# Kernel optimization log

Hardware: AMD Instinct MI355X
Metric: run time of the kernel (lower is better)

## Reference

```python
import jax, jax.numpy as jnp
import numpy as np
import math
from jax.scipy.special import gammaln

B, H, W = 32, 960, 960
BLOCK = 96  # official NIQE/NRQM block size

# AGGD shape-parameter lookup table (same grid as torch impl: 0.2..10 step 0.001)
_GAM_NP = np.arange(0.2, 10.0 + 1e-6, 0.001, dtype=np.float64)
_RG_NP = np.array([math.exp(2.0 * math.lgamma(2.0 / g) - math.lgamma(1.0 / g) - math.lgamma(3.0 / g)) for g in _GAM_NP], dtype=np.float32)
GAM = jnp.asarray(_GAM_NP.astype(np.float32))
RGAM = jnp.asarray(_RG_NP)

def _gauss_kernel(size, sigma):
    ax = np.arange(size, dtype=np.float64) - (size - 1) / 2.0
    xx, yy = np.meshgrid(ax, ax)
    k = np.exp(-(xx ** 2 + yy ** 2) / (2.0 * sigma ** 2))
    return (k / k.sum()).astype(np.float32)

K7 = jnp.asarray(_gauss_kernel(7, 7.0 / 6.0))[None, None]  # MSCN window
K3 = jnp.asarray(_gauss_kernel(3, 0.5))[None, None]        # pyramid / downsample kernel

def _conv_same(x, k, edge_pad):
    ph = k.shape[-1] // 2
    mode = 'edge' if edge_pad else 'constant'
    x = jnp.pad(x, ((0, 0), (0, 0), (ph, ph), (ph, ph)), mode=mode)
    return jax.lax.conv_general_dilated(x, k, (1, 1), 'VALID', dimension_numbers=('NCHW', 'OIHW', 'NCHW'))

def _normalize(img):
    # MSCN: (img - mu) / (sigma + 1), replicate padding
    mu = _conv_same(img, K7, True)
    sigma = jnp.sqrt(jnp.abs(_conv_same(img * img, K7, True) - mu * mu))
    return (img - mu) / (sigma + 1.0)

def _downsample(img):
    # gaussian blur (3x3, sigma 0.5, zero same-pad) + stride-2 decimation
    return _conv_same(img, K3, False)[:, :, ::2, ::2]

def _aggd(x):
    # x: [b, nb, h, w]; vectorized AGGD parameter estimation over all blocks
    hw = (-2, -1)
    x2 = x * x
    ml = (x < 0).astype(x.dtype)
    mr = (x > 0).astype(x.dtype)
    cl = jnp.maximum(ml.sum(hw), 1.0)
    cr = jnp.maximum(mr.sum(hw), 1.0)
    lstd = jnp.sqrt((x2 * ml).sum(hw) / cl)
    rstd = jnp.sqrt((x2 * mr).sum(hw) / cr)
    gh = lstd / jnp.maximum(rstd, 1e-12)
    rhat = jnp.mean(jnp.abs(x), hw) ** 2 / jnp.maximum(jnp.mean(x2, hw), 1e-12)
    rhn = rhat * (gh ** 3 + 1.0) * (gh + 1.0) / ((gh * gh + 1.0) ** 2)
    idx = jnp.argmin(jnp.abs(RGAM - rhn[..., None]), axis=-1)  # table lookup
    alpha = GAM[idx]
    conv = jnp.exp(0.5 * (gammaln(1.0 / alpha) - gammaln(3.0 / alpha)))
    return alpha, lstd * conv, rstd * conv

def _features(blocks):
    # 18 features per block: AGGD of block + AGGD of 4 shifted products
    alpha, bl, br = _aggd(blocks)
    feats = [alpha, (bl + br) / 2.0]
    for shift in ((0, 1), (1, 0), (1, 1), (1, -1)):
        sb = jnp.roll(blocks, shift, axis=(2, 3))
        a, l, r = _aggd(blocks * sb)
        mean = (r - l) * jnp.exp(gammaln(2.0 / a) - gammaln(1.0 / a))
        feats += [a, mean, l, r]
    return jnp.stack(feats, axis=-1)  # [b, nb, 18]

def _blocks(x, bs):
    b, _, h, w = x.shape
    nh, nw = h // bs, w // bs
    x = x[:, 0].reshape(b, nh, bs, nw, bs).transpose(0, 1, 3, 2, 4)
    return x.reshape(b, nh * nw, bs, bs)

def setup_inputs() -> dict:
    key = jax.random.key(0)
    k1, k2, k3 = jax.random.split(key, 3)
    X = jax.random.uniform(k1, (B, 1, H, W), jnp.float32) * 255.0
    mu_pris = jax.random.normal(k2, (36,), jnp.float32)
    A = jax.random.normal(k3, (36, 36), jnp.float32)
    cov_pris = A @ A.T / 36.0 + jnp.eye(36, dtype=jnp.float32)  # SPD pristine covariance
    return {"X": X, "mu_pris": mu_pris, "cov_pris": cov_pris}

def reference(X, mu_pris, cov_pris):
    feats = []
    img = X
    for scale in (1, 2):
        xn = _normalize(img)
        feats.append(_features(_blocks(xn, BLOCK // scale)))  # [b, 100, 18]
        if scale == 1:
            img = _downsample(img)
    d = jnp.concatenate(feats, axis=-1)  # [b, nb, 36]
    mu_dist = d.mean(axis=1)  # [b, 36]
    c = d - mu_dist[:, None, :]
    cov_dist = jnp.einsum('bnf,bng->bfg', c, c) / (d.shape[1] - 1)
    invcov = jnp.linalg.pinv((cov_pris[None] + cov_dist) / 2.0)
    diff = mu_pris[None] - mu_dist
    q = jnp.einsum('bf,bfg,bg->b', diff, invcov, diff)
    return jnp.sqrt(jnp.maximum(q, 0.0))
```

## Files before the change

kernel.cpp:

```cpp
#include <hip/hip_runtime.h>
#include <hip/hip_fp16.h>
#include <math.h>

#define NTAB 9801
typedef unsigned int uint;
typedef float f2v __attribute__((ext_vector_type(2)));
typedef _Float16 h2v __attribute__((ext_vector_type(2)));

struct WParams { float w1[7]; float wd[3]; };

__device__ inline __half2 u2h2(uint u) { return __builtin_bit_cast(__half2, u); }
__device__ inline float flo(uint u) { return __low2float(u2h2(u)); }
__device__ inline float fhi(uint u) { return __high2float(u2h2(u)); }
__device__ inline uint pkmul(uint a, uint b) { return __builtin_bit_cast(uint, __hmul2(u2h2(a), u2h2(b))); }
__device__ inline uint pack2(float a, float b) {
    return __builtin_bit_cast(uint, __builtin_amdgcn_cvt_pkrtz(a, b));
}
__device__ inline uint algn16(uint hi, uint lo) {
    return (uint)((((unsigned long long)hi << 32) | lo) >> 16);
}
__device__ inline float fdot2f(uint a, uint b, float c) {
    return __builtin_amdgcn_fdot2(__builtin_bit_cast(h2v, a), __builtin_bit_cast(h2v, b), c, false);
}
__device__ inline float rcpf(float x) { return __builtin_amdgcn_rcpf(x); }

template <int S, bool FUSE_DOWN, bool TABLES, typename TIN>
__global__ __launch_bounds__(256, 6) void mscn_col_k(const TIN* __restrict__ src,
                                                     uint* __restrict__ xn_out,
                                                     __half* __restrict__ down_out,
                                                     WParams wp,
                                                     float* __restrict__ rgam,
                                                     float* __restrict__ gam) {
    constexpr int ROW_W = 132, H_OUT = 42, H_IN = H_OUT + 6, RPT = H_OUT / 2;
    constexpr int NTX = (S + 255) / 256, NTY = (S + H_OUT - 1) / H_OUT;
    constexpr int NBLK = 32 * NTX * NTY;

    if constexpr (TABLES) {
        if (blockIdx.x >= (unsigned)NBLK) {
            int i = (blockIdx.x - NBLK) * 256 + threadIdx.x;
            if (i < NTAB) {
                double g = 0.2 + (double)i * 0.001;
                double v = exp(2.0 * lgamma(2.0 / g) - lgamma(1.0 / g) - lgamma(3.0 / g));
                rgam[i] = (float)v;
                gam[i]  = (float)g;
            }
            return;
        }
    }

    __shared__ uint tin[ROW_W * H_IN];

    const int tid = threadIdx.x;
    const int bid = blockIdx.x;
    const int b  = bid / (NTX * NTY);
    const int t2 = bid % (NTX * NTY);
    const int x0 = min((t2 / NTY) * 256, S - 256);
    const int y0 = min((t2 % NTY) * H_OUT, S - H_OUT);

    const float* w1 = wp.w1;
    uint wA[4], wB[4];
    wA[0] = pack2(0.f, w1[0]);   wA[1] = pack2(w1[1], w1[2]);
    wA[2] = pack2(w1[3], w1[4]); wA[3] = pack2(w1[5], w1[6]);
    wB[0] = pack2(w1[0], w1[1]); wB[1] = pack2(w1[2], w1[3]);
    wB[2] = pack2(w1[4], w1[5]); wB[3] = pack2(w1[6], 0.f);

    const TIN* img = src + (size_t)b * S * S;
    const bool interior = (x0 >= 4) && (x0 <= S - 260) && (y0 >= 3) && (y0 <= S - H_IN + 3);

    if (interior && sizeof(TIN) == 4) {
        const float4* base = reinterpret_cast<const float4*>((const float*)img + (size_t)(y0 - 3) * S + (x0 - 4));
        const int f4row = S / 4;
        for (int i = tid; i < 66 * H_IN; i += 256) {
            int r = i / 66, k = i - r * 66;
            float4 v = base[(size_t)r * f4row + k];
            tin[r * ROW_W + 2 * k]     = pack2(v.x, v.y);
            tin[r * ROW_W + 2 * k + 1] = pack2(v.z, v.w);
        }
    } else {
        for (int i = tid; i < ROW_W * H_IN; i += 256) {
            int r = i / ROW_W, w = i - r * ROW_W;
            int gy = y0 + r - 3; gy = gy < 0 ? 0 : (gy >= S ? S - 1 : gy);
            int c0 = x0 - 4 + 2 * w; c0 = c0 < 0 ? 0 : (c0 >= S ? S - 1 : c0);
            int c1 = x0 - 3 + 2 * w; c1 = c1 < 0 ? 0 : (c1 >= S ? S - 1 : c1);
            const TIN* rp = img + (size_t)gy * S;
            tin[i] = pack2((float)rp[c0], (float)rp[c1]);
        }
    }
    __syncthreads();

    const int g = tid >> 7, c = tid & 127;
    const int R0 = g * RPT;

    auto horiz = [&](int row, f2v& o1, f2v& o2) {
        const uint* pw = &tin[row * ROW_W + c];
        uint q0 = pw[0], q1 = pw[1], q2 = pw[2], q3 = pw[3], q4 = pw[4];
        uint p0 = pkmul(q0, q0), p1 = pkmul(q1, q1), p2 = pkmul(q2, q2),
             p3 = pkmul(q3, q3), p4 = pkmul(q4, q4);
        float s1A = fdot2f(q3, wA[3], fdot2f(q2, wA[2], fdot2f(q1, wA[1], fdot2f(q0, wA[0], 0.f))));
        float s2A = fdot2f(p3, wA[3], fdot2f(p2, wA[2], fdot2f(p1, wA[1], fdot2f(p0, wA[0], 0.f))));
        float s1B = fdot2f(q4, wB[3], fdot2f(q3, wB[2], fdot2f(q2, wB[1], fdot2f(q1, wB[0], 0.f))));
        float s2B = fdot2f(p4, wB[3], fdot2f(p3, wB[2], fdot2f(p2, wB[1], fdot2f(p1, wB[0], 0.f))));
        o1 = (f2v){s1A, s1B};
        o2 = (f2v){s2A, s2B};
    };

    f2v r1[7], r2[7];
#pragma unroll
    for (int ir = 0; ir < 6; ir++) horiz(R0 + ir, r1[ir], r2[ir]);

    uint* xnp = xn_out + ((((size_t)b * S + y0 + R0) * S + x0) >> 1) + c;
#pragma unroll
    for (int u = 0; u < RPT; u++) {
        horiz(R0 + u + 6, r1[(u + 6) % 7], r2[(u + 6) % 7]);
        f2v a1 = (f2v)(0.f), a2 = (f2v)(0.f);
#pragma unroll
        for (int dy = 0; dy < 7; dy++) {
            a1 += r1[(u + dy) % 7] * w1[dy];
            a2 += r2[(u + dy) % 7] * w1[dy];
        }
        uint qc = tin[(R0 + u + 3) * ROW_W + c + 2];
        float v0a = flo(qc), v0b = fhi(qc);
        float xa = (v0a - a1.x) * rcpf(sqrtf(fabsf(a2.x - a1.x * a1.x)) + 1.f);
        float xb = (v0b - a1.y) * rcpf(sqrtf(fabsf(a2.y - a1.y * a1.y)) + 1.f);
        xnp[(size_t)u * (S / 2)] = pack2(xa, xb);
    }

    if constexpr (FUSE_DOWN) {
        const float* wd = wp.wd;
        const int d = tid & 127, hf = tid >> 7;
        const int Xd = x0 / 2 + d;
        const float mL = (x0 + 2 * d - 1 >= 0) ? 1.f : 0.f;
#pragma unroll
        for (int jj = 0; jj <= RPT / 2; jj++) {
            int j = 2 * jj + hf;
            if (j >= RPT) continue;
            int Yd = y0 / 2 + j;
            float acc = 0.f;
#pragma unroll
            for (int a = 0; a < 3; a++) {
                int gy = 2 * Yd - 1 + a;
                if (gy < 0) continue;
                int tr = gy - y0 + 3;
                uint u1 = tin[tr * ROW_W + d + 1];
                uint u2 = tin[tr * ROW_W + d + 2];
                float rs = wd[0] * fhi(u1) * mL + wd[1] * flo(u2) + wd[2] * fhi(u2);
                acc += wd[a] * rs;
            }
            down_out[((size_t)b * (S / 2) + Yd) * (S / 2) + Xd] = __float2half(acc);
        }
    }
}

template <int BS>
__global__ __launch_bounds__(256) void feat2_k(const __half* __restrict__ xnimg, int S,
                                               const float* __restrict__ rgam,
                                               const float* __restrict__ gam,
                                               float* __restrict__ dfeat, int foff) {
    constexpr int WROW = BS / 2;
    constexpr int NWORD = BS * BS / 2;
    constexpr int NITER = (NWORD + 255) / 256;
    __shared__ uint xs[NWORD];
    __shared__ float red[4 * 20];
    __shared__ float tot[20];

    const int tid = threadIdx.x;
    const int b   = blockIdx.x / 100;
    const int blk = blockIdx.x % 100;
    const int by  = (blk / 10) * BS;
    const int bx  = (blk % 10) * BS;

    const uint* gw = (const uint*)xnimg;
    for (int i = tid; i < NWORD; i += 256) {
        int y = i / WROW, w = i - y * WROW;
        xs[i] = gw[((((size_t)b * S + by + y) * S + bx) >> 1) + w];
    }
    __syncthreads();

    float ssq[5], sab[5], ssg[5];
    uint  cnt[5];
#pragma unroll
    for (int v = 0; v < 5; v++) { ssq[v] = sab[v] = ssg[v] = 0.f; cnt[v] = 0u; }

    const uint ONE2 = 0x3C003C00u;

    for (int k = 0; k < NITER; k++) {
        int idx = tid + k * 256;
        if (idx * 2 < BS * BS) {
            int p0 = idx * 2;
            int y = p0 / BS;
            int x = p0 - y * BS;
            int w0i = x >> 1;
            int wm = w0i ? w0i - 1 : WROW - 1;
            int wp = (w0i + 1 == WROW) ? 0 : w0i + 1;
            int ym1 = y ? y - 1 : BS - 1;
            int rb = y * WROW, rbm = ym1 * WROW;
            uint V0 = xs[rb + w0i];
            uint WL = xs[rb + wm];
            uint AL = xs[rbm + wm];
            uint AC = xs[rbm + w0i];
            uint AR = xs[rbm + wp];
            uint vv[5];
            vv[0] = V0;
            vv[1] = pkmul(V0, algn16(V0, WL));
            vv[2] = pkmul(V0, AC);
            vv[3] = pkmul(V0, algn16(AC, AL));
            vv[4] = pkmul(V0, algn16(AR, AC));
#pragma unroll
            for (int v = 0; v < 5; v++) {
                uint av = vv[v] & 0x7FFF7FFFu;
                ssq[v] = fdot2f(vv[v], vv[v], ssq[v]);
                sab[v] = fdot2f(av, ONE2, sab[v]);
                ssg[v] = fdot2f(vv[v], av, ssg[v]);
                cnt[v] += (vv[v] >> 15) & 0x00010001u;
            }
        }
    }

    const int wid = tid >> 6, lane = tid & 63;
#pragma unroll
    for (int v = 0; v < 5; v++) {
        float a = ssq[v], bb = sab[v], cc = ssg[v];
        float dd = (float)((cnt[v] & 0xFFFFu) + (cnt[v] >> 16));
        for (int off = 32; off >= 1; off >>= 1) {
            a += __shfl_down(a, off); bb += __shfl_down(bb, off);
            cc += __shfl_down(cc, off); dd += __shfl_down(dd, off);
        }
        if (lane == 0) {
            red[wid * 20 + v]      = a;
            red[wid * 20 + 5 + v]  = bb;
            red[wid * 20 + 10 + v] = cc;
            red[wid * 20 + 15 + v] = dd;
        }
    }
    __syncthreads();
    if (tid < 20) tot[tid] = red[tid] + red[20 + tid] + red[40 + tid] + red[60 + tid];
    __syncthreads();

    if (tid < 5) {
        const int v = tid;
        const float N = (float)(BS * BS);
        float ssqv = tot[v], sabv = tot[5 + v], ssgv = tot[10 + v], clv = tot[15 + v];
        float sql = fmaxf(0.5f * (ssqv - ssgv), 0.f);
        float sqr = fmaxf(0.5f * (ssqv + ssgv), 0.f);
        float cl = fmaxf(clv, 1.f), cr = fmaxf(N - clv, 1.f);
        float lstd = sqrtf(sql / cl), rstd = sqrtf(sqr / cr);
        float gh = lstd / fmaxf(rstd, 1e-12f);
        float mabs = sabv / N, msq = ssqv / N;
        float rhat = (mabs * mabs) / fmaxf(msq, 1e-12f);
        float gh2 = gh * gh;
        float target = rhat * (gh * gh2 + 1.f) * (gh + 1.f) / ((gh2 + 1.f) * (gh2 + 1.f));

        int lo = 0, hi = NTAB - 1, j = NTAB;
        while (lo <= hi) {
            int mid = (lo + hi) >> 1;
            if (rgam[mid] >= target) { j = mid; hi = mid - 1; } else lo = mid + 1;
        }
        int i0 = j > 0 ? j - 1 : 0;
        int i1 = j < NTAB ? j : NTAB - 1;
        float d0 = fabsf(rgam[i0] - target);
        float d1 = fabsf(rgam[i1] - target);
        int bi = (d1 < d0) ? i1 : i0;

        float alpha = gam[bi];
        float conv  = expf(0.5f * (lgammaf(1.f / alpha) - lgammaf(3.f / alpha)));
        float bl = lstd * conv, br = rstd * conv;
        float* outp = dfeat + ((size_t)b * 100 + blk) * 36 + foff;
        if (v == 0) {
            outp[0] = alpha;
            outp[1] = 0.5f * (bl + br);
        } else {
            float mean = (br - bl) * expf(lgammaf(2.f / alpha) - lgammaf(1.f / alpha));
            int base = 2 + (v - 1) * 4;
            outp[base + 0] = alpha; outp[base + 1] = mean;
            outp[base + 2] = bl;    outp[base + 3] = br;
        }
    }
}

__global__ __launch_bounds__(256) void final_k(const float* __restrict__ dfeat,
                                               const float* __restrict__ mu_pris,
                                               const float* __restrict__ cov_pris,
                                               float* __restrict__ out) {
    __shared__ float  ds[3600];
    __shared__ float  mu[36];
    __shared__ double M[36][37];
    __shared__ double rhs[36];
    __shared__ double qacc;
    const int b = blockIdx.x, tid = threadIdx.x;
    const float* src = dfeat + (size_t)b * 3600;
    for (int i = tid; i < 3600; i += 256) ds[i] = src[i];
    __syncthreads();
    if (tid < 36) {
        float s = 0.f;
        for (int n = 0; n < 100; n++) s += ds[n * 36 + tid];
        mu[tid] = s / 100.f;
    }
    __syncthreads();
    for (int i = tid; i < 3600; i += 256) ds[i] -= mu[i % 36];
    if (tid < 36) rhs[tid] = (double)mu_pris[tid] - (double)mu[tid];
    if (tid == 0) qacc = 0.0;
    __syncthreads();
    for (int e = tid; e < 1296; e += 256) {
        int f = e / 36, g = e % 36;
        float s = 0.f;
        for (int n = 0; n < 100; n++) s += ds[n * 36 + f] * ds[n * 36 + g];
        M[f][g] = 0.5 * ((double)cov_pris[e] + (double)(s / 99.f));
    }
    __syncthreads();
    for (int j = 0; j < 36; j++) {
        if (tid == 0) qacc += rhs[j] * rhs[j] / M[j][j];
        int i = j + 1 + tid;
        if (i < 36) {
            double L = M[i][j] / M[j][j];
            for (int k = j; k < 36; k++) M[i][k] -= L * M[j][k];
            rhs[i] -= L * rhs[j];
        }
        __syncthreads();
    }
    if (tid == 0) out[b] = sqrtf((float)(qacc > 0.0 ? qacc : 0.0));
}

static WParams make_weights() {
    WParams p;
    double wt[7], s = 0.0; const double sg = 7.0 / 6.0;
    for (int i = 0; i < 7; i++) { double d = i - 3; wt[i] = exp(-d * d / (2.0 * sg * sg)); s += wt[i]; }
    for (int i = 0; i < 7; i++) p.w1[i] = (float)(wt[i] / s);
    double e1 = exp(-2.0), sd = 1.0 + 2.0 * e1;
    p.wd[0] = p.wd[2] = (float)(e1 / sd);
    p.wd[1] = (float)(1.0 / sd);
    return p;
}

extern "C" void kernel_launch(void* const* d_in, const int* in_sizes, int n_in,
                              void* d_out, int out_size, void* d_ws, size_t ws_size,
                              hipStream_t stream) {
    const float* X        = (const float*)d_in[0];
    const float* mu_pris  = (const float*)d_in[1];
    const float* cov_pris = (const float*)d_in[2];
    float* out = (float*)d_out;

    char* ws = (char*)d_ws;
    float*  rgam   = (float*)(ws);
    float*  gam    = (float*)(ws + 39424);
    float*  dfeat  = (float*)(ws + 78848);
    __half* xn960  = (__half*)(ws + 539648);
    __half* img480 = (__half*)(ws + 59522048);
    __half* xn480  = (__half*)(ws + 74267648);

    WParams wp = make_weights();

    constexpr int NB960 = 32 * 4 * 23;
    constexpr int TBLB  = (NTAB + 255) / 256;
    mscn_col_k<960, true,  true,  float ><<<NB960 + TBLB, 256, 0, stream>>>(
        X, (uint*)xn960, img480, wp, rgam, gam);
    mscn_col_k<480, false, false, __half><<<32 * 2 * 12, 256, 0, stream>>>(
        img480, (uint*)xn480, nullptr, wp, rgam, gam);
    feat2_k<96><<<3200, 256, 0, stream>>>(xn960, 960, rgam, gam, dfeat, 0);
    feat2_k<48><<<3200, 256, 0, stream>>>(xn480, 480, rgam, gam, dfeat, 18);
    final_k<<<32, 256, 0, stream>>>(dfeat, mu_pris, cov_pris, out);
}
```

Before: 223.2 us.

## Merge scale-2 MSCN with scale-1 features into one launch and vectorize loads

Refactors the MSCN and feature kernels into device bodies. The 480-scale MSCN and the 96-block feature extraction now share one launch, so independent work overlaps and one kernel boundary disappears. The MSCN tile height drops from 42 to 28 rows, raising block count and occupancy at the cost of more halo rows. Shared-memory stores and global loads are widened to uint2/uint4, the half-precision input path copies packed words directly, and the feature loop handles two words per thread. Heterogeneous blocks in the merged launch may balance unevenly.

```diff
diff --git a/kernel.cpp b/kernel.cpp
--- a/kernel.cpp
+++ b/kernel.cpp
@@ -24,34 +24,16 @@
 }
 __device__ inline float rcpf(float x) { return __builtin_amdgcn_rcpf(x); }
 
-template <int S, bool FUSE_DOWN, bool TABLES, typename TIN>
-__global__ __launch_bounds__(256, 6) void mscn_col_k(const TIN* __restrict__ src,
-                                                     uint* __restrict__ xn_out,
-                                                     __half* __restrict__ down_out,
-                                                     WParams wp,
-                                                     float* __restrict__ rgam,
-                                                     float* __restrict__ gam) {
-    constexpr int ROW_W = 132, H_OUT = 42, H_IN = H_OUT + 6, RPT = H_OUT / 2;
+template <int S, bool FUSE_DOWN, typename TIN>
+__device__ __forceinline__ void mscn_body(int bid, uint* tin,
+                                          const TIN* __restrict__ src,
+                                          uint* __restrict__ xn_out,
+                                          __half* __restrict__ down_out,
+                                          const WParams& wp) {
+    constexpr int ROW_W = 132, H_OUT = 28, H_IN = H_OUT + 6, RPT = H_OUT / 2;
     constexpr int NTX = (S + 255) / 256, NTY = (S + H_OUT - 1) / H_OUT;
-    constexpr int NBLK = 32 * NTX * NTY;
-
-    if constexpr (TABLES) {
-        if (blockIdx.x >= (unsigned)NBLK) {
-            int i = (blockIdx.x - NBLK) * 256 + threadIdx.x;
-            if (i < NTAB) {
-                double g = 0.2 + (double)i * 0.001;
-                double v = exp(2.0 * lgamma(2.0 / g) - lgamma(1.0 / g) - lgamma(3.0 / g));
-                rgam[i] = (float)v;
-                gam[i]  = (float)g;
-            }
-            return;
-        }
-    }
-
-    __shared__ uint tin[ROW_W * H_IN];
 
     const int tid = threadIdx.x;
-    const int bid = blockIdx.x;
     const int b  = bid / (NTX * NTY);
     const int t2 = bid % (NTX * NTY);
     const int x0 = min((t2 / NTY) * 256, S - 256);
@@ -67,23 +49,41 @@
     const TIN* img = src + (size_t)b * S * S;
     const bool interior = (x0 >= 4) && (x0 <= S - 260) && (y0 >= 3) && (y0 <= S - H_IN + 3);
 
-    if (interior && sizeof(TIN) == 4) {
-        const float4* base = reinterpret_cast<const float4*>((const float*)img + (size_t)(y0 - 3) * S + (x0 - 4));
-        const int f4row = S / 4;
-        for (int i = tid; i < 66 * H_IN; i += 256) {
-            int r = i / 66, k = i - r * 66;
-            float4 v = base[(size_t)r * f4row + k];
-            tin[r * ROW_W + 2 * k]     = pack2(v.x, v.y);
-            tin[r * ROW_W + 2 * k + 1] = pack2(v.z, v.w);
+    if constexpr (sizeof(TIN) == 4) {
+        if (interior) {
+            const float4* base = reinterpret_cast<const float4*>(
+                (const float*)img + (size_t)(y0 - 3) * S + (x0 - 4));
+            const int f4row = S / 4;
+            for (int i = tid; i < 66 * H_IN; i += 256) {
+                int r = i / 66, k = i - r * 66;
+                float4 v = base[(size_t)r * f4row + k];
+                uint2 pr; pr.x = pack2(v.x, v.y); pr.y = pack2(v.z, v.w);
+                *(uint2*)&tin[r * ROW_W + 2 * k] = pr;
+            }
+        } else {
+            for (int i = tid; i < ROW_W * H_IN; i += 256) {
+                int r = i / ROW_W, w = i - r * ROW_W;
+                int gy = y0 + r - 3; gy = gy < 0 ? 0 : (gy >= S ? S - 1 : gy);
+                int c0 = x0 - 4 + 2 * w; int c0c = c0 < 0 ? 0 : (c0 >= S ? S - 1 : c0);
+                int c1 = c0 + 1;         int c1c = c1 < 0 ? 0 : (c1 >= S ? S - 1 : c1);
+                const TIN* rp = img + (size_t)gy * S;
+                tin[i] = pack2((float)rp[c0c], (float)rp[c1c]);
+            }
         }
     } else {
+        const uint* gw = (const uint*)img;
         for (int i = tid; i < ROW_W * H_IN; i += 256) {
             int r = i / ROW_W, w = i - r * ROW_W;
             int gy = y0 + r - 3; gy = gy < 0 ? 0 : (gy >= S ? S - 1 : gy);
-            int c0 = x0 - 4 + 2 * w; c0 = c0 < 0 ? 0 : (c0 >= S ? S - 1 : c0);
-            int c1 = x0 - 3 + 2 * w; c1 = c1 < 0 ? 0 : (c1 >= S ? S - 1 : c1);
-            const TIN* rp = img + (size_t)gy * S;
-            tin[i] = pack2((float)rp[c0], (float)rp[c1]);
+            int c0 = x0 - 4 + 2 * w;
+            if (c0 >= 0 && c0 + 1 < S) {
+                tin[i] = gw[((size_t)gy * S + c0) >> 1];
+            } else {
+                int c0c = c0 < 0 ? 0 : (c0 >= S ? S - 1 : c0);
+                int c1c = (c0 + 1) < 0 ? 0 : ((c0 + 1) >= S ? S - 1 : c0 + 1);
+                const TIN* rp = img + (size_t)gy * S;
+                tin[i] = pack2((float)rp[c0c], (float)rp[c1c]);
+            }
         }
     }
     __syncthreads();
@@ -131,9 +131,8 @@
         const int Xd = x0 / 2 + d;
         const float mL = (x0 + 2 * d - 1 >= 0) ? 1.f : 0.f;
 #pragma unroll
-        for (int jj = 0; jj <= RPT / 2; jj++) {
+        for (int jj = 0; jj < RPT / 2; jj++) {
             int j = 2 * jj + hf;
-            if (j >= RPT) continue;
             int Yd = y0 / 2 + j;
             float acc = 0.f;
 #pragma unroll
@@ -152,27 +151,29 @@
 }
 
 template <int BS>
-__global__ __launch_bounds__(256) void feat2_k(const __half* __restrict__ xnimg, int S,
-                                               const float* __restrict__ rgam,
-                                               const float* __restrict__ gam,
-                                               float* __restrict__ dfeat, int foff) {
+__device__ __forceinline__ void feat2_body(int bid, uint* xs, float* red, float* tot,
+                                           const __half* __restrict__ xnimg, int S,
+                                           const float* __restrict__ rgam,
+                                           const float* __restrict__ gam,
+                                           float* __restrict__ dfeat, int foff) {
     constexpr int WROW = BS / 2;
     constexpr int NWORD = BS * BS / 2;
-    constexpr int NITER = (NWORD + 255) / 256;
-    __shared__ uint xs[NWORD];
-    __shared__ float red[4 * 20];
-    __shared__ float tot[20];
+    constexpr int PAIRS = NWORD / 2;
+    constexpr int PPR = WROW / 2;
 
     const int tid = threadIdx.x;
-    const int b   = blockIdx.x / 100;
-    const int blk = blockIdx.x % 100;
+    const int b   = bid / 100;
+    const int blk = bid % 100;
     const int by  = (blk / 10) * BS;
     const int bx  = (blk % 10) * BS;
 
     const uint* gw = (const uint*)xnimg;
-    for (int i = tid; i < NWORD; i += 256) {
-        int y = i / WROW, w = i - y * WROW;
-        xs[i] = gw[((((size_t)b * S + by + y) * S + bx) >> 1) + w];
+    uint4* xs4 = (uint4*)xs;
+    constexpr int NW4 = NWORD / 4;
+    constexpr int W4R = WROW / 4;
+    for (int i = tid; i < NW4; i += 256) {
+        int y = i / W4R, k = i - y * W4R;
+        xs4[i] = *(const uint4*)&gw[((((size_t)b * S + by + y) * S + bx) >> 1) + 4 * k];
     }
     __syncthreads();
 
@@ -183,35 +184,36 @@
 
     const uint ONE2 = 0x3C003C00u;
 
-    for (int k = 0; k < NITER; k++) {
+    for (int k = 0; k < (PAIRS + 255) / 256; k++) {
         int idx = tid + k * 256;
-        if (idx * 2 < BS * BS) {
-            int p0 = idx * 2;
-            int y = p0 / BS;
-            int x = p0 - y * BS;
-            int w0i = x >> 1;
-            int wm = w0i ? w0i - 1 : WROW - 1;
-            int wp = (w0i + 1 == WROW) ? 0 : w0i + 1;
-            int ym1 = y ? y - 1 : BS - 1;
-            int rb = y * WROW, rbm = ym1 * WROW;
-            uint V0 = xs[rb + w0i];
-            uint WL = xs[rb + wm];
-            uint AL = xs[rbm + wm];
-            uint AC = xs[rbm + w0i];
-            uint AR = xs[rbm + wp];
-            uint vv[5];
-            vv[0] = V0;
-            vv[1] = pkmul(V0, algn16(V0, WL));
-            vv[2] = pkmul(V0, AC);
-            vv[3] = pkmul(V0, algn16(AC, AL));
-            vv[4] = pkmul(V0, algn16(AR, AC));
+        if (idx < PAIRS) {
+            int y  = idx / PPR;
+            int pr = idx - y * PPR;
+            int w0 = pr * 2;
+            int rb = y * WROW, rbm = (y ? y - 1 : BS - 1) * WROW;
+            uint2 V = *(const uint2*)&xs[rb + w0];
+            uint WL  = xs[rb  + (w0 ? w0 - 1 : WROW - 1)];
+            uint2 A = *(const uint2*)&xs[rbm + w0];
+            uint AL  = xs[rbm + (w0 ? w0 - 1 : WROW - 1)];
+            uint AR  = xs[rbm + ((w0 + 2 == WROW) ? 0 : w0 + 2)];
+            uint vA[5], vB[5];
+            vA[0] = V.x;
+            vA[1] = pkmul(V.x, algn16(V.x, WL));
+            vA[2] = pkmul(V.x, A.x);
+            vA[3] = pkmul(V.x, algn16(A.x, AL));
+            vA[4] = pkmul(V.x, algn16(A.y, A.x));
+            vB[0] = V.y;
+            vB[1] = pkmul(V.y, algn16(V.y, V.x));
+            vB[2] = pkmul(V.y, A.y);
+            vB[3] = pkmul(V.y, algn16(A.y, A.x));
+            vB[4] = pkmul(V.y, algn16(AR, A.y));
 #pragma unroll
             for (int v = 0; v < 5; v++) {
-                uint av = vv[v] & 0x7FFF7FFFu;
-                ssq[v] = fdot2f(vv[v], vv[v], ssq[v]);
-                sab[v] = fdot2f(av, ONE2, sab[v]);
-                ssg[v] = fdot2f(vv[v], av, ssg[v]);
-                cnt[v] += (vv[v] >> 15) & 0x00010001u;
+                uint aA = vA[v] & 0x7FFF7FFFu, aB = vB[v] & 0x7FFF7FFFu;
+                ssq[v] = fdot2f(vB[v], vB[v], fdot2f(vA[v], vA[v], ssq[v]));
+                sab[v] = fdot2f(aB, ONE2, fdot2f(aA, ONE2, sab[v]));
+                ssg[v] = fdot2f(vB[v], aB, fdot2f(vA[v], aA, ssg[v]));
+                cnt[v] += ((vA[v] >> 15) & 0x00010001u) + ((vB[v] >> 15) & 0x00010001u);
             }
         }
     }
@@ -277,6 +279,55 @@
     }
 }
 
+__global__ __launch_bounds__(256, 8) void mscnA_k(const float* __restrict__ X,
+                                                  uint* __restrict__ xn960,
+                                                  __half* __restrict__ img480,
+                                                  WParams wp,
+                                                  float* __restrict__ rgam,
+                                                  float* __restrict__ gam) {
+    constexpr int NBLK = 32 * 4 * 35;
+    if (blockIdx.x >= (unsigned)NBLK) {
+        int i = (blockIdx.x - NBLK) * 256 + threadIdx.x;
+        if (i < NTAB) {
+            double g = 0.2 + (double)i * 0.001;
+            double v = exp(2.0 * lgamma(2.0 / g) - lgamma(1.0 / g) - lgamma(3.0 / g));
+            rgam[i] = (float)v;
+            gam[i]  = (float)g;
+        }
+        return;
+    }
+    __shared__ __align__(16) uint tin[132 * 34];
+    mscn_body<960, true, float>(blockIdx.x, tin, X, xn960, img480, wp);
+}
+
+__global__ __launch_bounds__(256, 8) void launchB_k(const __half* __restrict__ img480,
+                                                    uint* __restrict__ xn480,
+                                                    const __half* __restrict__ xn960,
+                                                    WParams wp,
+                                                    const float* __restrict__ rgam,
+                                                    const float* __restrict__ gam,
+                                                    float* __restrict__ dfeat) {
+    constexpr int NB480 = 32 * 2 * 18;
+    __shared__ __align__(16) uint smem[4608 + 100];
+    if (blockIdx.x < (unsigned)NB480) {
+        mscn_body<480, false, __half>(blockIdx.x, smem, img480, xn480, nullptr, wp);
+    } else {
+        float* red = (float*)(smem + 4608);
+        float* tot = red + 80;
+        feat2_body<96>(blockIdx.x - NB480, smem, red, tot, xn960, 960, rgam, gam, dfeat, 0);
+    }
+}
+
+__global__ __launch_bounds__(256, 8) void feat48_k(const __half* __restrict__ xn480,
+                                                   const float* __restrict__ rgam,
+                                                   const float* __restrict__ gam,
+                                                   float* __restrict__ dfeat) {
+    __shared__ __align__(16) uint smem[1152 + 100];
+    float* red = (float*)(smem + 1152);
+    float* tot = red + 80;
+    feat2_body<48>(blockIdx.x, smem, red, tot, xn480, 480, rgam, gam, dfeat, 18);
+}
+
 __global__ __launch_bounds__(256) void final_k(const float* __restrict__ dfeat,
                                                const float* __restrict__ mu_pris,
                                                const float* __restrict__ cov_pris,
@@ -349,13 +400,11 @@
 
     WParams wp = make_weights();
 
-    constexpr int NB960 = 32 * 4 * 23;
+    constexpr int NB960 = 32 * 4 * 35;
     constexpr int TBLB  = (NTAB + 255) / 256;
-    mscn_col_k<960, true,  true,  float ><<<NB960 + TBLB, 256, 0, stream>>>(
-        X, (uint*)xn960, img480, wp, rgam, gam);
-    mscn_col_k<480, false, false, __half><<<32 * 2 * 12, 256, 0, stream>>>(
-        img480, (uint*)xn480, nullptr, wp, rgam, gam);
-    feat2_k<96><<<3200, 256, 0, stream>>>(xn960, 960, rgam, gam, dfeat, 0);
-    feat2_k<48><<<3200, 256, 0, stream>>>(xn480, 480, rgam, gam, dfeat, 18);
+    mscnA_k<<<NB960 + TBLB, 256, 0, stream>>>(X, (uint*)xn960, img480, wp, rgam, gam);
+    launchB_k<<<32 * 2 * 18 + 3200, 256, 0, stream>>>(img480, (uint*)xn480, xn960, wp,
+                                                      rgam, gam, dfeat);
+    feat48_k<<<3200, 256, 0, stream>>>(xn480, rgam, gam, dfeat);
     final_k<<<32, 256, 0, stream>>>(dfeat, mu_pris, cov_pris, out);
 }
```

After: 207.1 us. -7.2%, faster.
